# Optimization experiments

Hardware: AMD Instinct MI355X
Metric: run time of the kernel (lower is better)

Reference implementation:

```python
import jax, jax.numpy as jnp
import numpy as np

B, N, M, D = 8, 4096, 4096, 3

def setup_inputs() -> dict:
    key = jax.random.key(0)
    ks = jax.random.split(key, 6)
    return {
        "X_pred": jax.random.normal(ks[0], (B, N, D), dtype=jnp.float32),
        "X_true": jax.random.normal(ks[1], (B, M, D), dtype=jnp.float32),
        "R_pred": jax.random.normal(ks[2], (B, D, D), dtype=jnp.float32),
        "t_pred": jax.random.normal(ks[3], (B, D), dtype=jnp.float32),
        "R_true": jax.random.normal(ks[4], (B, D, D), dtype=jnp.float32),
        "t_true": jax.random.normal(ks[5], (B, D), dtype=jnp.float32),
        "temperature": jnp.asarray(0.1, dtype=jnp.float32),
    }

def reference(X_pred, X_true, R_pred, t_pred, R_true, t_true, temperature):
    # Rigid transforms: x' = R x + t
    Xp = jnp.einsum('bij,bnj->bni', R_pred, X_pred) + t_pred[:, None, :]  # (B,N,D)
    Xt = jnp.einsum('bij,bmj->bmi', R_true, X_true) + t_true[:, None, :]  # (B,M,D)
    # Squared pairwise distances: |a|^2 + |b|^2 - 2 a.b  (== cdist(p=2)**2)
    sq_p = jnp.sum(Xp * Xp, axis=-1)  # (B,N)
    sq_t = jnp.sum(Xt * Xt, axis=-1)  # (B,M)
    dist_sq = sq_p[:, :, None] + sq_t[:, None, :] - 2.0 * jnp.einsum('bnd,bmd->bnm', Xp, Xt)
    dist_sq = jnp.maximum(dist_sq, 0.0)  # (B,N,M)
    soft_alignment = jax.nn.softmax(-dist_sq / temperature, axis=-1)
    weighted_distances = jnp.sum(soft_alignment * dist_sq, axis=-1)  # (B,N)
    return jnp.mean(weighted_distances)
```

## Files before the change

kernel.cpp:

```cpp
#include <hip/hip_runtime.h>


#define B_    8
#define N_    4096
#define M_    4096
#define NWAVE 8
#define BLOCK 512
#define ROWS  512
#define RPL   8
#define MSPL  8
#define QCH   (M_ / MSPL)
#define WQ    (QCH / NWAVE)
#define LOG2E 1.4426950408889634f
#define LN2   0.6931471805599453f
#define NEGBIG -3.0e38f

__global__ __launch_bounds__(BLOCK, 4) void softfape_main(
    const float* __restrict__ X_pred, const float* __restrict__ X_true,
    const float* __restrict__ R_pred, const float* __restrict__ t_pred,
    const float* __restrict__ R_true, const float* __restrict__ t_true,
    const float* __restrict__ temp,
    float4* __restrict__ Pg)
{
    __shared__ float4 Q[QCH];
    __shared__ float  Lp[NWAVE][ROWS];
    __shared__ float  Sp[NWAVE][ROWS];
    __shared__ float  Mp[NWAVE][ROWS];

    const int tid  = threadIdx.x;
    const int wave = tid >> 6;
    const int lane = tid & 63;
    const int x    = blockIdx.x;
    const int ms   = x & 7;
    const int rg   = (x >> 3) & 7;
    const int b    = x >> 6;

    const float T   = temp[0];
    const float c   = LOG2E / T;
    const float m2c = -2.0f * c;

    if (tid < QCH / 2) {
        const float g00 = R_true[b*9+0], g01 = R_true[b*9+1], g02 = R_true[b*9+2];
        const float g10 = R_true[b*9+3], g11 = R_true[b*9+4], g12 = R_true[b*9+5];
        const float g20 = R_true[b*9+6], g21 = R_true[b*9+7], g22 = R_true[b*9+8];
        const float u0  = t_true[b*3+0], u1 = t_true[b*3+1], u2 = t_true[b*3+2];
        const float2* xt = (const float2*)(X_true + ((size_t)b * M_ + ms * QCH) * 3);
        const float2 f0 = xt[3*tid+0], f1 = xt[3*tid+1], f2 = xt[3*tid+2];
        {
            const float y0 = fmaf(g00, f0.x, fmaf(g01, f0.y, fmaf(g02, f1.x, u0)));
            const float y1 = fmaf(g10, f0.x, fmaf(g11, f0.y, fmaf(g12, f1.x, u1)));
            const float y2 = fmaf(g20, f0.x, fmaf(g21, f0.y, fmaf(g22, f1.x, u2)));
            const float nn = fmaf(y0, y0, fmaf(y1, y1, y2 * y2));
            Q[2*tid]   = make_float4(m2c*y0, m2c*y1, m2c*y2, c*nn);
        }
        {
            const float y0 = fmaf(g00, f1.y, fmaf(g01, f2.x, fmaf(g02, f2.y, u0)));
            const float y1 = fmaf(g10, f1.y, fmaf(g11, f2.x, fmaf(g12, f2.y, u1)));
            const float y2 = fmaf(g20, f1.y, fmaf(g21, f2.x, fmaf(g22, f2.y, u2)));
            const float nn = fmaf(y0, y0, fmaf(y1, y1, y2 * y2));
            Q[2*tid+1] = make_float4(m2c*y0, m2c*y1, m2c*y2, c*nn);
        }
    }

    float px[RPL], py[RPL], pz[RPL], sh[RPL];
    {
        const float h00 = R_pred[b*9+0], h01 = R_pred[b*9+1], h02 = R_pred[b*9+2];
        const float h10 = R_pred[b*9+3], h11 = R_pred[b*9+4], h12 = R_pred[b*9+5];
        const float h20 = R_pred[b*9+6], h21 = R_pred[b*9+7], h22 = R_pred[b*9+8];
        const float v0 = t_pred[b*3+0], v1 = t_pred[b*3+1], v2 = t_pred[b*3+2];
        const float4* xp = (const float4*)(X_pred + ((size_t)b * N_ + rg * ROWS + lane * RPL) * 3);
        float f[24];
        #pragma unroll
        for (int i = 0; i < 6; ++i) *(float4*)&f[4*i] = xp[i];
        #pragma unroll
        for (int r = 0; r < RPL; ++r) {
            const float rx = f[3*r], ry = f[3*r+1], rz = f[3*r+2];
            px[r] = fmaf(h00, rx, fmaf(h01, ry, fmaf(h02, rz, v0)));
            py[r] = fmaf(h10, rx, fmaf(h11, ry, fmaf(h12, rz, v1)));
            pz[r] = fmaf(h20, rx, fmaf(h21, ry, fmaf(h22, rz, v2)));
            sh[r] = -c * fmaf(px[r], px[r], fmaf(py[r], py[r], pz[r] * pz[r]));
        }
    }

    __syncthreads();

    const float4* __restrict__ Qw = Q + wave * WQ;

    float L[RPL], S[RPL], mx[RPL];
    #pragma unroll
    for (int r = 0; r < RPL; ++r) { L[r] = 0.0f; S[r] = 0.0f; mx[r] = NEGBIG; }
    for (int k0 = 0; k0 < WQ; k0 += 8) {
        float4 qv[8];
        #pragma unroll
        for (int j = 0; j < 8; ++j) qv[j] = Qw[k0 + j];
        #pragma unroll
        for (int j2 = 0; j2 < 4; ++j2) {
            const float4 q0 = qv[2*j2], q1 = qv[2*j2+1];
            #pragma unroll
            for (int r = 0; r < RPL; ++r) {
                const float A0   = fmaf(q0.x, px[r], fmaf(q0.y, py[r], fmaf(q0.z, pz[r], q0.w)));
                const float A1   = fmaf(q1.x, px[r], fmaf(q1.y, py[r], fmaf(q1.z, pz[r], q1.w)));
                const float arg0 = sh[r] - A0;
                const float arg1 = sh[r] - A1;
                const float w0   = __builtin_amdgcn_exp2f(arg0);
                const float w1   = __builtin_amdgcn_exp2f(arg1);
                L[r] += w0;
                L[r] += w1;
                S[r]  = fmaf(w0, arg0, S[r]);
                S[r]  = fmaf(w1, arg1, S[r]);
                mx[r] = fmaxf(fmaxf(mx[r], arg0), arg1);
            }
        }
    }
    *(float4*)&Lp[wave][RPL*lane]     = make_float4(L[0], L[1], L[2], L[3]);
    *(float4*)&Lp[wave][RPL*lane + 4] = make_float4(L[4], L[5], L[6], L[7]);
    *(float4*)&Sp[wave][RPL*lane]     = make_float4(S[0], S[1], S[2], S[3]);
    *(float4*)&Sp[wave][RPL*lane + 4] = make_float4(S[4], S[5], S[6], S[7]);
    *(float4*)&Mp[wave][RPL*lane]     = make_float4(mx[0], mx[1], mx[2], mx[3]);
    *(float4*)&Mp[wave][RPL*lane + 4] = make_float4(mx[4], mx[5], mx[6], mx[7]);
    __syncthreads();

    {
        float Lr = 0.0f, Sr = 0.0f, mw = Mp[0][tid];
        #pragma unroll
        for (int w2 = 0; w2 < NWAVE; ++w2) { Lr += Lp[w2][tid]; Sr += Sp[w2][tid]; }
        #pragma unroll
        for (int w2 = 1; w2 < NWAVE; ++w2) mw = fmaxf(mw, Mp[w2][tid]);
        const size_t row = (size_t)b * N_ + rg * ROWS + tid;
        Pg[row * MSPL + ms] = make_float4(0.0f, Lr, Sr, mw);
    }
}

__global__ __launch_bounds__(256) void softfape_finalize(
    const float4* __restrict__ Pg, const float* __restrict__ temp,
    float* __restrict__ out)
{
    __shared__ float ws4[4];
    const int tid = threadIdx.x;
    const size_t row = (size_t)blockIdx.x * 256 + tid;

    float4 P[MSPL];
    #pragma unroll
    for (int i = 0; i < MSPL; ++i) P[i] = Pg[row * MSPL + i];

    float m = P[0].x;
    float mw = P[0].w;
    #pragma unroll
    for (int i = 1; i < MSPL; ++i) { m = fminf(m, P[i].x); mw = fmaxf(mw, P[i].w); }

    float L = 0.0f, SA = 0.0f;
    #pragma unroll
    for (int i = 0; i < MSPL; ++i) {
        const float dm = m - P[i].x;
        const float f  = __builtin_amdgcn_exp2f(dm);
        L  = fmaf(P[i].y, f, L);
        SA = fmaf(f, fmaf(dm, P[i].y, P[i].z), SA);
    }
    float wd = (L > 0.0f) ? (m - SA / L) : -mw;

    wd += __shfl_xor(wd, 1);  wd += __shfl_xor(wd, 2);  wd += __shfl_xor(wd, 4);
    wd += __shfl_xor(wd, 8);  wd += __shfl_xor(wd, 16); wd += __shfl_xor(wd, 32);
    if ((tid & 63) == 0) ws4[tid >> 6] = wd;
    __syncthreads();
    if (tid == 0) {
        const float s = ws4[0] + ws4[1] + ws4[2] + ws4[3];
        const float scale = temp[0] * LN2 / ((float)B_ * (float)N_);
        atomicAdd(out, s * scale);
    }
}

extern "C" void kernel_launch(void* const* d_in, const int* in_sizes, int n_in,
                              void* d_out, int out_size, void* d_ws, size_t ws_size,
                              hipStream_t stream) {
    const float* X_pred = (const float*)d_in[0];
    const float* X_true = (const float*)d_in[1];
    const float* R_pred = (const float*)d_in[2];
    const float* t_pred = (const float*)d_in[3];
    const float* R_true = (const float*)d_in[4];
    const float* t_true = (const float*)d_in[5];
    const float* temp   = (const float*)d_in[6];
    float* out = (float*)d_out;

    float4* Pg = (float4*)d_ws;

    hipMemsetAsync(out, 0, sizeof(float), stream);

    softfape_main<<<dim3(B_ * (N_ / ROWS) * MSPL), BLOCK, 0, stream>>>(
        X_pred, X_true, R_pred, t_pred, R_true, t_true, temp, Pg);

    softfape_finalize<<<dim3((B_ * N_) / 256), 256, 0, stream>>>(Pg, temp, out);
}
```

Measured before the change: 95.75 us.

## Shrink blocks to 256 threads, split M 16 ways, store partials column-major

The main kernel now uses 256-thread blocks with 4 rows per lane and 16 M-splits, giving 2048 blocks that target 8 resident blocks per CU. The goal is better occupancy and lower register pressure in the exp-heavy inner loop. The partial-results layout changes from row-major to split-major so finalize reads are coalesced, and the unused per-split max offset is removed, which simplifies the finalize math. In exchange the finalize kernel reads twice as many partials, and each block repeats the per-batch setup more often.

```diff
diff --git a/kernel.cpp b/kernel.cpp
--- a/kernel.cpp
+++ b/kernel.cpp
@@ -4,18 +4,19 @@
 #define B_    8
 #define N_    4096
 #define M_    4096
-#define NWAVE 8
-#define BLOCK 512
-#define ROWS  512
-#define RPL   8
-#define MSPL  8
+#define NWAVE 4
+#define BLOCK 256
+#define ROWS  256
+#define RPL   4
+#define MSPL  16
 #define QCH   (M_ / MSPL)
 #define WQ    (QCH / NWAVE)
+#define BN    (B_ * N_)
 #define LOG2E 1.4426950408889634f
 #define LN2   0.6931471805599453f
 #define NEGBIG -3.0e38f
 
-__global__ __launch_bounds__(BLOCK, 4) void softfape_main(
+__global__ __launch_bounds__(BLOCK, 8) void softfape_main(
     const float* __restrict__ X_pred, const float* __restrict__ X_true,
     const float* __restrict__ R_pred, const float* __restrict__ t_pred,
     const float* __restrict__ R_true, const float* __restrict__ t_true,
@@ -31,35 +32,26 @@
     const int wave = tid >> 6;
     const int lane = tid & 63;
     const int x    = blockIdx.x;
-    const int ms   = x & 7;
-    const int rg   = (x >> 3) & 7;
-    const int b    = x >> 6;
+    const int ms   = x & 15;
+    const int rg   = (x >> 4) & 15;
+    const int b    = x >> 8;
 
     const float T   = temp[0];
     const float c   = LOG2E / T;
     const float m2c = -2.0f * c;
 
-    if (tid < QCH / 2) {
+    {
         const float g00 = R_true[b*9+0], g01 = R_true[b*9+1], g02 = R_true[b*9+2];
         const float g10 = R_true[b*9+3], g11 = R_true[b*9+4], g12 = R_true[b*9+5];
         const float g20 = R_true[b*9+6], g21 = R_true[b*9+7], g22 = R_true[b*9+8];
         const float u0  = t_true[b*3+0], u1 = t_true[b*3+1], u2 = t_true[b*3+2];
-        const float2* xt = (const float2*)(X_true + ((size_t)b * M_ + ms * QCH) * 3);
-        const float2 f0 = xt[3*tid+0], f1 = xt[3*tid+1], f2 = xt[3*tid+2];
-        {
-            const float y0 = fmaf(g00, f0.x, fmaf(g01, f0.y, fmaf(g02, f1.x, u0)));
-            const float y1 = fmaf(g10, f0.x, fmaf(g11, f0.y, fmaf(g12, f1.x, u1)));
-            const float y2 = fmaf(g20, f0.x, fmaf(g21, f0.y, fmaf(g22, f1.x, u2)));
-            const float nn = fmaf(y0, y0, fmaf(y1, y1, y2 * y2));
-            Q[2*tid]   = make_float4(m2c*y0, m2c*y1, m2c*y2, c*nn);
-        }
-        {
-            const float y0 = fmaf(g00, f1.y, fmaf(g01, f2.x, fmaf(g02, f2.y, u0)));
-            const float y1 = fmaf(g10, f1.y, fmaf(g11, f2.x, fmaf(g12, f2.y, u1)));
-            const float y2 = fmaf(g20, f1.y, fmaf(g21, f2.x, fmaf(g22, f2.y, u2)));
-            const float nn = fmaf(y0, y0, fmaf(y1, y1, y2 * y2));
-            Q[2*tid+1] = make_float4(m2c*y0, m2c*y1, m2c*y2, c*nn);
-        }
+        const float* xt = X_true + ((size_t)b * M_ + ms * QCH + tid) * 3;
+        const float rx = xt[0], ry = xt[1], rz = xt[2];
+        const float y0 = fmaf(g00, rx, fmaf(g01, ry, fmaf(g02, rz, u0)));
+        const float y1 = fmaf(g10, rx, fmaf(g11, ry, fmaf(g12, rz, u1)));
+        const float y2 = fmaf(g20, rx, fmaf(g21, ry, fmaf(g22, rz, u2)));
+        const float nn = fmaf(y0, y0, fmaf(y1, y1, y2 * y2));
+        Q[tid] = make_float4(m2c*y0, m2c*y1, m2c*y2, c*nn);
     }
 
     float px[RPL], py[RPL], pz[RPL], sh[RPL];
@@ -69,15 +61,15 @@
         const float h20 = R_pred[b*9+6], h21 = R_pred[b*9+7], h22 = R_pred[b*9+8];
         const float v0 = t_pred[b*3+0], v1 = t_pred[b*3+1], v2 = t_pred[b*3+2];
         const float4* xp = (const float4*)(X_pred + ((size_t)b * N_ + rg * ROWS + lane * RPL) * 3);
-        float f[24];
-        #pragma unroll
-        for (int i = 0; i < 6; ++i) *(float4*)&f[4*i] = xp[i];
+        const float4 a0 = xp[0], a1 = xp[1], a2 = xp[2];
+        const float rx[4] = {a0.x, a0.w, a1.z, a2.y};
+        const float ry[4] = {a0.y, a1.x, a1.w, a2.z};
+        const float rz[4] = {a0.z, a1.y, a2.x, a2.w};
         #pragma unroll
         for (int r = 0; r < RPL; ++r) {
-            const float rx = f[3*r], ry = f[3*r+1], rz = f[3*r+2];
-            px[r] = fmaf(h00, rx, fmaf(h01, ry, fmaf(h02, rz, v0)));
-            py[r] = fmaf(h10, rx, fmaf(h11, ry, fmaf(h12, rz, v1)));
-            pz[r] = fmaf(h20, rx, fmaf(h21, ry, fmaf(h22, rz, v2)));
+            px[r] = fmaf(h00, rx[r], fmaf(h01, ry[r], fmaf(h02, rz[r], v0)));
+            py[r] = fmaf(h10, rx[r], fmaf(h11, ry[r], fmaf(h12, rz[r], v1)));
+            pz[r] = fmaf(h20, rx[r], fmaf(h21, ry[r], fmaf(h22, rz[r], v2)));
             sh[r] = -c * fmaf(px[r], px[r], fmaf(py[r], py[r], pz[r] * pz[r]));
         }
     }
@@ -89,12 +81,12 @@
     float L[RPL], S[RPL], mx[RPL];
     #pragma unroll
     for (int r = 0; r < RPL; ++r) { L[r] = 0.0f; S[r] = 0.0f; mx[r] = NEGBIG; }
-    for (int k0 = 0; k0 < WQ; k0 += 8) {
-        float4 qv[8];
+    for (int k0 = 0; k0 < WQ; k0 += 4) {
+        float4 qv[4];
         #pragma unroll
-        for (int j = 0; j < 8; ++j) qv[j] = Qw[k0 + j];
+        for (int j = 0; j < 4; ++j) qv[j] = Qw[k0 + j];
         #pragma unroll
-        for (int j2 = 0; j2 < 4; ++j2) {
+        for (int j2 = 0; j2 < 2; ++j2) {
             const float4 q0 = qv[2*j2], q1 = qv[2*j2+1];
             #pragma unroll
             for (int r = 0; r < RPL; ++r) {
@@ -112,22 +104,21 @@
             }
         }
     }
-    *(float4*)&Lp[wave][RPL*lane]     = make_float4(L[0], L[1], L[2], L[3]);
-    *(float4*)&Lp[wave][RPL*lane + 4] = make_float4(L[4], L[5], L[6], L[7]);
-    *(float4*)&Sp[wave][RPL*lane]     = make_float4(S[0], S[1], S[2], S[3]);
-    *(float4*)&Sp[wave][RPL*lane + 4] = make_float4(S[4], S[5], S[6], S[7]);
-    *(float4*)&Mp[wave][RPL*lane]     = make_float4(mx[0], mx[1], mx[2], mx[3]);
-    *(float4*)&Mp[wave][RPL*lane + 4] = make_float4(mx[4], mx[5], mx[6], mx[7]);
+    *(float4*)&Lp[wave][RPL*lane] = make_float4(L[0], L[1], L[2], L[3]);
+    *(float4*)&Sp[wave][RPL*lane] = make_float4(S[0], S[1], S[2], S[3]);
+    *(float4*)&Mp[wave][RPL*lane] = make_float4(mx[0], mx[1], mx[2], mx[3]);
     __syncthreads();
 
     {
-        float Lr = 0.0f, Sr = 0.0f, mw = Mp[0][tid];
+        float Lr = Lp[0][tid], Sr = Sp[0][tid], mw = Mp[0][tid];
         #pragma unroll
-        for (int w2 = 0; w2 < NWAVE; ++w2) { Lr += Lp[w2][tid]; Sr += Sp[w2][tid]; }
-        #pragma unroll
-        for (int w2 = 1; w2 < NWAVE; ++w2) mw = fmaxf(mw, Mp[w2][tid]);
+        for (int w2 = 1; w2 < NWAVE; ++w2) {
+            Lr += Lp[w2][tid];
+            Sr += Sp[w2][tid];
+            mw  = fmaxf(mw, Mp[w2][tid]);
+        }
         const size_t row = (size_t)b * N_ + rg * ROWS + tid;
-        Pg[row * MSPL + ms] = make_float4(0.0f, Lr, Sr, mw);
+        Pg[(size_t)ms * BN + row] = make_float4(Lr, Sr, mw, 0.0f);
     }
 }
 
@@ -139,24 +130,16 @@
     const int tid = threadIdx.x;
     const size_t row = (size_t)blockIdx.x * 256 + tid;
 
-    float4 P[MSPL];
-    #pragma unroll
-    for (int i = 0; i < MSPL; ++i) P[i] = Pg[row * MSPL + i];
-
-    float m = P[0].x;
-    float mw = P[0].w;
-    #pragma unroll
-    for (int i = 1; i < MSPL; ++i) { m = fminf(m, P[i].x); mw = fmaxf(mw, P[i].w); }
-
-    float L = 0.0f, SA = 0.0f;
+    float L = 0.0f, SA = 0.0f, mw = NEGBIG;
     #pragma unroll
     for (int i = 0; i < MSPL; ++i) {
-        const float dm = m - P[i].x;
-        const float f  = __builtin_amdgcn_exp2f(dm);
-        L  = fmaf(P[i].y, f, L);
-        SA = fmaf(f, fmaf(dm, P[i].y, P[i].z), SA);
+        const float4 P = Pg[(size_t)i * BN + row];
+        L  += P.x;
+        SA += P.y;
+        mw  = fmaxf(mw, P.z);
     }
-    float wd = (L > 0.0f) ? (m - SA / L) : -mw;
+    const float wd0 = (L > 0.0f) ? (-SA / L) : -mw;
+    float wd = wd0;
 
     wd += __shfl_xor(wd, 1);  wd += __shfl_xor(wd, 2);  wd += __shfl_xor(wd, 4);
     wd += __shfl_xor(wd, 8);  wd += __shfl_xor(wd, 16); wd += __shfl_xor(wd, 32);
@@ -188,5 +171,5 @@
     softfape_main<<<dim3(B_ * (N_ / ROWS) * MSPL), BLOCK, 0, stream>>>(
         X_pred, X_true, R_pred, t_pred, R_true, t_true, temp, Pg);
 
-    softfape_finalize<<<dim3((B_ * N_) / 256), 256, 0, stream>>>(Pg, temp, out);
+    softfape_finalize<<<dim3(BN / 256), 256, 0, stream>>>(Pg, temp, out);
 }
```

Result: slower. 99.23 us (+3.6%).
